# Kernel tuning notes

Measured on AMD Instinct MI355X. Metric: run time of the kernel, lower is better.

Reference implementation:

```python
import jax, jax.numpy as jnp
import numpy as np

E = 512
H = 8
DH = E // H
LN_EPS = 1e-5


def setup_inputs() -> dict:
    key = jax.random.key(0)
    ks = jax.random.split(key, 8)
    s = 1.0 / np.sqrt(E)
    return {
        "query": jax.random.normal(ks[0], (2, 2048, E), jnp.float32),
        "key_value": jax.random.normal(ks[1], (2, 4096, E), jnp.float32),
        "Wq": jax.random.normal(ks[2], (E, E), jnp.float32) * s,
        "bq": jnp.zeros((E,), jnp.float32),
        "Wk": jax.random.normal(ks[3], (E, E), jnp.float32) * s,
        "bk": jnp.zeros((E,), jnp.float32),
        "Wv": jax.random.normal(ks[4], (E, E), jnp.float32) * s,
        "bv": jnp.zeros((E,), jnp.float32),
        "Wo": jax.random.normal(ks[5], (E, E), jnp.float32) * s,
        "bo": jnp.zeros((E,), jnp.float32),
        "ln_gamma": jnp.ones((E,), jnp.float32),
        "ln_beta": jnp.zeros((E,), jnp.float32),
    }


def reference(query, key_value, Wq, bq, Wk, bk, Wv, bv, Wo, bo, ln_gamma, ln_beta):
    B, Lq, _ = query.shape
    Lk = key_value.shape[1]
    # Projections (torch Linear: x @ W.T + b)
    q = (query @ Wq.T + bq).reshape(B, Lq, H, DH)
    k = (key_value @ Wk.T + bk).reshape(B, Lk, H, DH)
    v = (key_value @ Wv.T + bv).reshape(B, Lk, H, DH)
    scale = 1.0 / np.sqrt(DH).astype(np.float32)
    scores = jnp.einsum("bqhd,bkhd->bhqk", q, k) * scale  # [B,H,Lq,Lk]
    attn = jax.nn.softmax(scores, axis=-1)
    ctx = jnp.einsum("bhqk,bkhd->bqhd", attn, v).reshape(B, Lq, E)
    attn_out = ctx @ Wo.T + bo
    # residual + LayerNorm (dropout is identity in eval)
    x = query + attn_out
    mu = jnp.mean(x, axis=-1, keepdims=True)
    var = jnp.mean(jnp.square(x - mu), axis=-1, keepdims=True)
    return (x - mu) * jax.lax.rsqrt(var + LN_EPS) * ln_gamma + ln_beta
```

## Files before the change

### kernel.cpp

```cpp
#include <hip/hip_runtime.h>
#include <hip/hip_bf16.h>

typedef __bf16 bf16;
typedef __bf16 bf16x8 __attribute__((ext_vector_type(8)));
typedef __bf16 bf16x4 __attribute__((ext_vector_type(4)));
typedef float f32x4 __attribute__((ext_vector_type(4)));
typedef float f32x16 __attribute__((ext_vector_type(16)));
typedef unsigned int u32x4 __attribute__((ext_vector_type(4)));

#define MFMA16(a, b, c) __builtin_amdgcn_mfma_f32_16x16x32_bf16((a), (b), (c), 0, 0, 0)
#define MFMA32(a, b, c) __builtin_amdgcn_mfma_f32_32x32x16_bf16((a), (b), (c), 0, 0, 0)

constexpr int LQ = 2048, LK = 4096, E = 512, H = 8, DH = 64;
#define QSCALE 0.1803368801111137f

#if __has_builtin(__builtin_amdgcn_exp2f)
#define EXP2(x) __builtin_amdgcn_exp2f(x)
#else
#define EXP2(x) __expf(0.6931471805599453f * (x))
#endif

__device__ __forceinline__ bf16x8 ld8(const bf16* p) { return *(const bf16x8*)p; }

__global__ __launch_bounds__(256) void cvt4_kernel(
    const float* __restrict__ w0, const float* __restrict__ w1,
    const float* __restrict__ w2, const float* __restrict__ w3,
    bf16* __restrict__ dst) {
  const float* srcs[4] = {w0, w1, w2, w3};
  const float* src = srcs[blockIdx.y];
  bf16* d = dst + (size_t)blockIdx.y * 262144;
  int i = (blockIdx.x * 256 + threadIdx.x) * 4;
  f32x4 v = *(const f32x4*)(src + i);
  bf16x4 o;
  for (int j = 0; j < 4; ++j) o[j] = (bf16)v[j];
  *(bf16x4*)(d + i) = o;
}

__global__ __launch_bounds__(256) void proj_gemm_kernel(
    const float* __restrict__ query, const float* __restrict__ kv,
    const bf16* __restrict__ Wall,
    const float* __restrict__ bq, const float* __restrict__ bk,
    const float* __restrict__ bv,
    bf16* __restrict__ qproj, bf16* __restrict__ kproj, bf16* __restrict__ vt) {
  __shared__ __align__(16) char smem[36864];
  typedef bf16 RowT[72];
  RowT* smA = (RowT*)smem;
  RowT* smB = (RowT*)(smem + 18432);

  const int tid = threadIdx.x;
  const int lane = tid & 63, wave = tid >> 6;
  const int lrow = lane & 15, quad = lane >> 4;
  const int wm = wave & 1, wn = wave >> 1;

  int x = blockIdx.x, z, mt;
  if (x < 32) { z = 0; mt = x; }
  else if (x < 96) { z = 1; mt = x - 32; }
  else { z = 2; mt = x - 96; }
  const float* A = ((z == 0) ? query : kv) + (size_t)mt * 128 * E;
  const bf16* W = Wall + (size_t)z * 262144;
  const float* bias = (z == 0) ? bq : (z == 1) ? bk : bv;
  const int n0 = blockIdx.y * 128;

  const int arow = tid >> 4, acol = tid & 15;
  const int brow = tid >> 3, bcol = tid & 7;

  f32x4 pa[8];
  bf16x8 pb[4];
#define LOAD_T(t)                                                             \
  {                                                                           \
    for (int p = 0; p < 8; ++p)                                               \
      pa[p] = *(const f32x4*)(A + (size_t)(p * 16 + arow) * E + (t) * 64 +    \
                              acol * 4);                                      \
    for (int p = 0; p < 4; ++p)                                               \
      pb[p] = ld8(W + (size_t)(n0 + p * 32 + brow) * E + (t) * 64 + bcol * 8);\
  }
#define STORE_T()                                                             \
  {                                                                           \
    for (int p = 0; p < 8; ++p) {                                             \
      bf16x4 av;                                                              \
      for (int e = 0; e < 4; ++e) av[e] = (bf16)pa[p][e];                     \
      *(bf16x4*)&smA[p * 16 + arow][acol * 4] = av;                           \
    }                                                                         \
    for (int p = 0; p < 4; ++p)                                               \
      *(bf16x8*)&smB[p * 32 + brow][bcol * 8] = pb[p];                        \
  }

  LOAD_T(0);
  STORE_T();
  LOAD_T(1);
  __syncthreads();

  f32x4 acc[4][4] = {};
  for (int t = 0; t < 8; ++t) {
    bf16x8 af[2][4], bfr[2][4];
    for (int ks = 0; ks < 2; ++ks)
      for (int i = 0; i < 4; ++i)
        af[ks][i] = ld8(&smA[wm * 64 + 16 * i + lrow][ks * 32 + quad * 8]);
    for (int ks = 0; ks < 2; ++ks)
      for (int c = 0; c < 4; ++c)
        bfr[ks][c] = ld8(&smB[wn * 64 + 16 * c + lrow][ks * 32 + quad * 8]);
    for (int ks = 0; ks < 2; ++ks)
      for (int i = 0; i < 4; ++i)
        for (int c = 0; c < 4; ++c)
          acc[i][c] = MFMA16(af[ks][i], bfr[ks][c], acc[i][c]);
    if (t < 7) {
      __syncthreads();
      STORE_T();
      if (t < 6) LOAD_T(t + 2);
      __syncthreads();
    }
  }
#undef LOAD_T
#undef STORE_T

  const float qsc = (z == 0) ? QSCALE : 1.f;
  float bvl[4];
  for (int c = 0; c < 4; ++c) bvl[c] = bias[n0 + wn * 64 + 16 * c + lrow];
  __syncthreads();
  bf16* Cs = (bf16*)smem;
  for (int i = 0; i < 4; ++i)
    for (int c = 0; c < 4; ++c)
      for (int r = 0; r < 4; ++r) {
        int row = wm * 64 + 16 * i + 4 * quad + r;
        int col = wn * 64 + 16 * c + lrow;
        bf16 val = (bf16)((acc[i][c][r] + bvl[c]) * qsc);
        if (z < 2) Cs[row * 136 + col] = val;
        else       Cs[col * 136 + row] = val;
      }
  __syncthreads();
  const int rr = tid >> 1, hh = tid & 1;
  if (z == 0) {
    bf16* dstp = qproj + (size_t)(mt * 128 + rr) * E + n0 + hh * 64;
    for (int j = 0; j < 8; ++j)
      *(bf16x8*)(dstp + j * 8) = *(bf16x8*)&Cs[rr * 136 + hh * 64 + j * 8];
  } else if (z == 1) {
    int mtg = mt * 128 + rr;
    int b2 = mtg >> 12, kk = mtg & 4095;
    int t32 = kk >> 5, l31 = kk & 31;
    int bh2 = b2 * 8 + (n0 >> 6) + hh;
    bf16* dstp = kproj + (size_t)bh2 * 262144 + (size_t)t32 * 2048 + l31 * 8;
    for (int j = 0; j < 8; ++j)
      *(bf16x8*)(dstp + j * 256) = *(bf16x8*)&Cs[rr * 136 + hh * 64 + j * 8];
  } else {
    int m0g = mt * 128, b2 = m0g >> 12, kk0 = m0g & 4095;
    int ng = n0 + rr, hd = ng >> 6, d = ng & 63;
    int bh2 = b2 * 8 + hd, dt = d >> 5, l31 = d & 31;
    bf16* dstp = vt + (size_t)bh2 * 262144 + dt * 1024 + l31 * 8;
    for (int j = 0; j < 8; ++j) {
      int kk = kk0 + hh * 64 + 8 * j;
      int t32 = kk >> 5, s = (kk >> 4) & 1, hi2 = (kk >> 3) & 1;
      *(bf16x8*)(dstp + (size_t)t32 * 2048 + s * 512 + hi2 * 256) =
          *(bf16x8*)&Cs[rr * 136 + hh * 64 + j * 8];
    }
  }
}

__global__ __launch_bounds__(256, 2) void attn_kernel(
    const bf16* __restrict__ qp, const bf16* __restrict__ kfg,
    const bf16* __restrict__ vfg, bf16* __restrict__ ctx) {
  const int tid = threadIdx.x;
  const int lane = tid & 63, wave = tid >> 6;
  const int l31 = lane & 31, hi = lane >> 5;
  const int hw = blockIdx.x;
  const int xcd = hw & 7, ii = hw >> 3;
  const int bh = xcd * 2 + (ii >> 5), qt = ii & 31;
  const int b = bh >> 3, h = bh & 7;
  const int q0 = qt * 64;

  __shared__ __align__(16) char smem[34816];

  bf16x8 qf[2][4];
  for (int t = 0; t < 2; ++t)
    for (int st = 0; st < 4; ++st)
      qf[t][st] = ld8(qp + (size_t)(b * LQ + q0 + 32 * t + l31) * E + h * DH +
                      st * 16 + hi * 8);

  float lp[2] = {0.f, 0.f};
  f32x16 acc[2][2] = {};

  const size_t tb = ((size_t)bh * 128 + wave * 32) * 2048;
  const bf16* kb = kfg + tb + hi * 256 + l31 * 8;
  const bf16* vb = vfg + tb + hi * 256 + l31 * 8;

#define LOADT(kf_, vf_, it)                                          \
  {                                                                  \
    const bf16* kp_ = kb + (size_t)(it) * 2048;                      \
    kf_[0] = ld8(kp_);                                               \
    kf_[1] = ld8(kp_ + 512);                                         \
    kf_[2] = ld8(kp_ + 1024);                                        \
    kf_[3] = ld8(kp_ + 1536);                                        \
    const bf16* vp_ = vb + (size_t)(it) * 2048;                      \
    vf_[0] = ld8(vp_);                                               \
    vf_[1] = ld8(vp_ + 512);                                         \
    vf_[2] = ld8(vp_ + 1024);                                        \
    vf_[3] = ld8(vp_ + 1536);                                        \
  }

#define COMPUTE(kf_, vf_)                                            \
  _Pragma("unroll")                                                  \
  for (int t = 0; t < 2; ++t) {                                      \
    f32x16 s_ = {};                                                  \
    __builtin_amdgcn_s_setprio(1);                                   \
    s_ = MFMA32(kf_[0], qf[t][0], s_);                               \
    s_ = MFMA32(kf_[1], qf[t][1], s_);                               \
    s_ = MFMA32(kf_[2], qf[t][2], s_);                               \
    s_ = MFMA32(kf_[3], qf[t][3], s_);                               \
    __builtin_amdgcn_s_setprio(0);                                   \
    unsigned w_[4][2];                                               \
    _Pragma("unroll")                                                \
    for (int t4 = 0; t4 < 4; ++t4)                                   \
      _Pragma("unroll")                                              \
      for (int u = 0; u < 2; ++u) {                                  \
        float e0 = EXP2(s_[4 * t4 + 2 * u]);                         \
        float e1 = EXP2(s_[4 * t4 + 2 * u + 1]);                     \
        lp[t] += e0;                                                 \
        lp[t] += e1;                                                 \
        asm("v_cvt_pk_bf16_f32 %0, %1, %2"                           \
            : "=v"(w_[t4][u])                                        \
            : "v"(e0), "v"(e1));                                     \
      }                                                              \
    bf16x8 paf[2];                                                   \
    _Pragma("unroll")                                                \
    for (int s = 0; s < 2; ++s) {                                    \
      unsigned a0 = w_[2 * s][0], b0 = w_[2 * s + 1][0];             \
      unsigned a1 = w_[2 * s][1], b1 = w_[2 * s + 1][1];             \
      asm("v_permlane32_swap_b32 %0, %1" : "+v"(a0), "+v"(b0));      \
      asm("v_permlane32_swap_b32 %0, %1" : "+v"(a1), "+v"(b1));      \
      u32x4 pw_ = {a0, a1, b0, b1};                                  \
      paf[s] = *(bf16x8*)&pw_;                                       \
    }                                                                \
    __builtin_amdgcn_s_setprio(1);                                   \
    acc[t][0] = MFMA32(paf[0], vf_[0], acc[t][0]);                   \
    acc[t][0] = MFMA32(paf[1], vf_[1], acc[t][0]);                   \
    acc[t][1] = MFMA32(paf[0], vf_[2], acc[t][1]);                   \
    acc[t][1] = MFMA32(paf[1], vf_[3], acc[t][1]);                   \
    __builtin_amdgcn_s_setprio(0);                                   \
  }

  bf16x8 kfA[4], vfA[4], kfB[4], vfB[4];
  LOADT(kfA, vfA, 0);
  for (int it = 0; it < 32; it += 2) {
    LOADT(kfB, vfB, it + 1);
    COMPUTE(kfA, vfA);
    if (it + 2 < 32) LOADT(kfA, vfA, it + 2);
    COMPUTE(kfB, vfB);
  }
#undef LOADT
#undef COMPUTE

  for (int t = 0; t < 2; ++t) lp[t] += __shfl_xor(lp[t], 32);

  float* F = (float*)smem;
  float* Lr = (float*)(smem + 33792);
  if (hi == 0) {
    Lr[wave * 64 + l31] = lp[0];
    Lr[wave * 64 + 32 + l31] = lp[1];
  }
#pragma unroll
  for (int t = 0; t < 2; ++t)
#pragma unroll
    for (int r = 0; r < 16; ++r) {
      int q = 32 * t + (r & 3) + 8 * (r >> 2) + 4 * hi;
      F[(wave * 64 + q) * 33 + l31] = acc[t][0][r];
    }
  __syncthreads();
  const int mq = tid >> 2, d0 = (tid & 3) * 8;
  float ls = Lr[mq] + Lr[64 + mq] + Lr[128 + mq] + Lr[192 + mq];
  const float inv = 1.f / ls;
  {
    float o[8] = {};
#pragma unroll
    for (int w2 = 0; w2 < 4; ++w2) {
      const float* Fr = &F[(w2 * 64 + mq) * 33 + d0];
      for (int j = 0; j < 8; ++j) o[j] += Fr[j];
    }
    bf16x8 ov;
    for (int j = 0; j < 8; ++j) ov[j] = (bf16)(o[j] * inv);
    *(bf16x8*)(ctx + (size_t)(b * LQ + q0 + mq) * E + h * DH + d0) = ov;
  }
  __syncthreads();
#pragma unroll
  for (int t = 0; t < 2; ++t)
#pragma unroll
    for (int r = 0; r < 16; ++r) {
      int q = 32 * t + (r & 3) + 8 * (r >> 2) + 4 * hi;
      F[(wave * 64 + q) * 33 + l31] = acc[t][1][r];
    }
  __syncthreads();
  {
    float o[8] = {};
#pragma unroll
    for (int w2 = 0; w2 < 4; ++w2) {
      const float* Fr = &F[(w2 * 64 + mq) * 33 + d0];
      for (int j = 0; j < 8; ++j) o[j] += Fr[j];
    }
    bf16x8 ov;
    for (int j = 0; j < 8; ++j) ov[j] = (bf16)(o[j] * inv);
    *(bf16x8*)(ctx + (size_t)(b * LQ + q0 + mq) * E + h * DH + 32 + d0) = ov;
  }
}

__global__ __launch_bounds__(256) void outgemm_kernel(
    const bf16* __restrict__ Cx, const bf16* __restrict__ Wo,
    float* __restrict__ y) {
  __shared__ bf16 smA[2][128][72];
  __shared__ bf16 smB[2][128][72];
  const int tid = threadIdx.x;
  const int lane = tid & 63, wave = tid >> 6;
  const int lrow = lane & 15, quad = lane >> 4;
  const int wm = wave & 1, wn = wave >> 1;
  const int m0 = blockIdx.x * 128, n0 = blockIdx.y * 128;
  const bf16* A = Cx + (size_t)m0 * E;

  const int srow = tid >> 3, schunk = tid & 7;

  bf16x8 pa[4], pb[4];
#define LOAD_T(t)                                                             \
  {                                                                           \
    for (int p = 0; p < 4; ++p)                                               \
      pa[p] = ld8(A + (size_t)(p * 32 + srow) * E + (t) * 64 + schunk * 8);   \
    for (int p = 0; p < 4; ++p)                                               \
      pb[p] = ld8(Wo + (size_t)(n0 + p * 32 + srow) * E + (t) * 64 +          \
                  schunk * 8);                                                \
  }
#define STORE_T(bs)                                                           \
  {                                                                           \
    for (int p = 0; p < 4; ++p)                                               \
      *(bf16x8*)&smA[bs][p * 32 + srow][schunk * 8] = pa[p];                  \
    for (int p = 0; p < 4; ++p)                                               \
      *(bf16x8*)&smB[bs][p * 32 + srow][schunk * 8] = pb[p];                  \
  }

  LOAD_T(0);
  STORE_T(0);
  LOAD_T(1);
  __syncthreads();

  f32x4 acc[4][4] = {};
  for (int t = 0; t < 8; ++t) {
    const int bs = t & 1;
    bf16x8 af[2][4], bfr[2][4];
    for (int ks = 0; ks < 2; ++ks)
      for (int i = 0; i < 4; ++i)
        af[ks][i] = ld8(&smA[bs][wm * 64 + 16 * i + lrow][ks * 32 + quad * 8]);
    for (int ks = 0; ks < 2; ++ks)
      for (int c = 0; c < 4; ++c)
        bfr[ks][c] = ld8(&smB[bs][wn * 64 + 16 * c + lrow][ks * 32 + quad * 8]);
    for (int ks = 0; ks < 2; ++ks)
      for (int i = 0; i < 4; ++i)
        for (int c = 0; c < 4; ++c)
          acc[i][c] = MFMA16(af[ks][i], bfr[ks][c], acc[i][c]);
    if (t < 7) {
      STORE_T(bs ^ 1);
      if (t < 6) LOAD_T(t + 2);
    }
    __syncthreads();
  }
#undef LOAD_T
#undef STORE_T

  for (int i = 0; i < 4; ++i)
    for (int c = 0; c < 4; ++c)
      for (int r = 0; r < 4; ++r) {
        int row = m0 + wm * 64 + 16 * i + 4 * quad + r;
        int col = n0 + wn * 64 + 16 * c + lrow;
        y[(size_t)row * E + col] = acc[i][c][r];
      }
}

__global__ __launch_bounds__(256) void ln_kernel(
    const float* __restrict__ y, const float* __restrict__ resid,
    const float* __restrict__ bo, const float* __restrict__ gamma,
    const float* __restrict__ beta, float* __restrict__ out) {
  const int tid = threadIdx.x;
  const int lane = tid & 63, wave = tid >> 6;
  const int row = blockIdx.x * 4 + wave;
  const int c0 = lane * 8;

  const float* yr = y + (size_t)row * E + c0;
  const float* rr = resid + (size_t)row * E + c0;
  f32x4 y0 = *(const f32x4*)yr, y1 = *(const f32x4*)(yr + 4);
  f32x4 r0 = *(const f32x4*)rr, r1 = *(const f32x4*)(rr + 4);
  f32x4 b0 = *(const f32x4*)(bo + c0), b1 = *(const f32x4*)(bo + c0 + 4);

  float xv[8];
  float s1 = 0.f, s2 = 0.f;
  for (int j = 0; j < 4; ++j) {
    xv[j] = y0[j] + r0[j] + b0[j];
    xv[4 + j] = y1[j] + r1[j] + b1[j];
  }
  for (int j = 0; j < 8; ++j) {
    s1 += xv[j];
    s2 += xv[j] * xv[j];
  }
  for (int off = 1; off < 64; off <<= 1) {
    s1 += __shfl_xor(s1, off);
    s2 += __shfl_xor(s2, off);
  }
  const float mean = s1 * (1.f / 512.f);
  const float var = s2 * (1.f / 512.f) - mean * mean;
  const float rstd = rsqrtf(var + 1e-5f);

  f32x4 g0 = *(const f32x4*)(gamma + c0), g1 = *(const f32x4*)(gamma + c0 + 4);
  f32x4 t0 = *(const f32x4*)(beta + c0), t1 = *(const f32x4*)(beta + c0 + 4);
  f32x4 o0, o1;
  for (int j = 0; j < 4; ++j) {
    o0[j] = (xv[j] - mean) * rstd * g0[j] + t0[j];
    o1[j] = (xv[4 + j] - mean) * rstd * g1[j] + t1[j];
  }
  float* op = out + (size_t)row * E + c0;
  *(f32x4*)op = o0;
  *(f32x4*)(op + 4) = o1;
}

extern "C" void kernel_launch(void* const* d_in, const int* in_sizes, int n_in,
                              void* d_out, int out_size, void* d_ws, size_t ws_size,
                              hipStream_t stream) {
  const float* query     = (const float*)d_in[0];
  const float* key_value = (const float*)d_in[1];
  const float* Wq = (const float*)d_in[2];
  const float* bq = (const float*)d_in[3];
  const float* Wk = (const float*)d_in[4];
  const float* bk = (const float*)d_in[5];
  const float* Wv = (const float*)d_in[6];
  const float* bv = (const float*)d_in[7];
  const float* Wo = (const float*)d_in[8];
  const float* bo = (const float*)d_in[9];
  const float* gamma = (const float*)d_in[10];
  const float* beta  = (const float*)d_in[11];
  float* out = (float*)d_out;

  bf16* Wb    = (bf16*)d_ws;
  bf16* Wob   = Wb + (size_t)3 * 262144;
  bf16* qproj = Wb + (size_t)4 * 262144;
  bf16* kproj = qproj + (size_t)4096 * 512;
  bf16* vt    = kproj + (size_t)8192 * 512;
  float* y    = (float*)(vt + (size_t)8192 * 512);

  cvt4_kernel<<<dim3(256, 4), 256, 0, stream>>>(Wq, Wk, Wv, Wo, Wb);
  proj_gemm_kernel<<<dim3(160, 4), 256, 0, stream>>>(
      query, key_value, Wb, bq, bk, bv, qproj, kproj, vt);
  attn_kernel<<<512, 256, 0, stream>>>(qproj, kproj, vt, qproj );
  outgemm_kernel<<<dim3(32, 4), 256, 0, stream>>>(qproj, Wob, y);
  ln_kernel<<<1024, 256, 0, stream>>>(y, query, bo, gamma, beta, out);
}
```

Measured before the change: 167.3 us.

## Pre-swizzle weights into MFMA fragment layout and load B directly from global

The weight conversion kernel now writes bf16 weights in an MFMA-fragment-ordered layout so that each lane can load its B operand straight from global memory into registers. This removes the B shared-memory staging in both projection and output GEMMs. The projection GEMM gains double-buffered A tiles with one barrier per iteration and a 3-block occupancy hint. The output GEMM halves its M tile to 64 rows to double the grid size. The trade-off is more global/L2 traffic for weights, since each wave re-reads its B fragments instead of sharing them through LDS.

```diff
diff --git a/kernel.cpp b/kernel.cpp
--- a/kernel.cpp
+++ b/kernel.cpp
@@ -22,21 +22,28 @@
 
 __device__ __forceinline__ bf16x8 ld8(const bf16* p) { return *(const bf16x8*)p; }
 
-__global__ __launch_bounds__(256) void cvt4_kernel(
+__global__ __launch_bounds__(256) void cvt4f_kernel(
     const float* __restrict__ w0, const float* __restrict__ w1,
     const float* __restrict__ w2, const float* __restrict__ w3,
     bf16* __restrict__ dst) {
+  int gid = blockIdx.x * 256 + threadIdx.x;
+  int z = gid >> 15;
+  int rem = gid & 32767;
+  int row = rem >> 6, cc = rem & 63;
   const float* srcs[4] = {w0, w1, w2, w3};
-  const float* src = srcs[blockIdx.y];
-  bf16* d = dst + (size_t)blockIdx.y * 262144;
-  int i = (blockIdx.x * 256 + threadIdx.x) * 4;
-  f32x4 v = *(const f32x4*)(src + i);
-  bf16x4 o;
-  for (int j = 0; j < 4; ++j) o[j] = (bf16)v[j];
-  *(bf16x4*)(d + i) = o;
-}
-
-__global__ __launch_bounds__(256) void proj_gemm_kernel(
+  const float* s = srcs[z] + row * 512 + cc * 8;
+  f32x4 v0 = *(const f32x4*)s, v1 = *(const f32x4*)(s + 4);
+  bf16x8 o;
+  for (int j = 0; j < 4; ++j) {
+    o[j] = (bf16)v0[j];
+    o[4 + j] = (bf16)v1[j];
+  }
+  int n16 = row >> 4, lrow = row & 15, k32 = cc >> 2, quad = cc & 3;
+  int slot = (n16 * 16 + k32) * 64 + quad * 16 + lrow;
+  *(bf16x8*)(dst + (size_t)z * 262144 + (size_t)slot * 8) = o;
+}
+
+__global__ __launch_bounds__(256, 3) void proj_gemm_kernel(
     const float* __restrict__ query, const float* __restrict__ kv,
     const bf16* __restrict__ Wall,
     const float* __restrict__ bq, const float* __restrict__ bk,
@@ -44,8 +51,8 @@
     bf16* __restrict__ qproj, bf16* __restrict__ kproj, bf16* __restrict__ vt) {
   __shared__ __align__(16) char smem[36864];
   typedef bf16 RowT[72];
-  RowT* smA = (RowT*)smem;
-  RowT* smB = (RowT*)(smem + 18432);
+  RowT* smA0 = (RowT*)smem;
+  RowT* smA1 = (RowT*)(smem + 18432);
 
   const int tid = threadIdx.x;
   const int lane = tid & 63, wave = tid >> 6;
@@ -57,66 +64,67 @@
   else if (x < 96) { z = 1; mt = x - 32; }
   else { z = 2; mt = x - 96; }
   const float* A = ((z == 0) ? query : kv) + (size_t)mt * 128 * E;
-  const bf16* W = Wall + (size_t)z * 262144;
   const float* bias = (z == 0) ? bq : (z == 1) ? bk : bv;
   const int n0 = blockIdx.y * 128;
 
+  const bf16* wb = Wall + (size_t)z * 262144 + (size_t)lane * 8;
+  const int n16b = (n0 >> 4) + wn * 4;
+
   const int arow = tid >> 4, acol = tid & 15;
-  const int brow = tid >> 3, bcol = tid & 7;
 
   f32x4 pa[8];
-  bf16x8 pb[4];
-#define LOAD_T(t)                                                             \
+  bf16x8 bfr[2][4];
+#define LOAD_A(t)                                                             \
+  for (int p = 0; p < 8; ++p)                                                 \
+    pa[p] = *(const f32x4*)(A + (size_t)(p * 16 + arow) * E + (t) * 64 +      \
+                            acol * 4);
+#define STORE_A(bs)                                                           \
   {                                                                           \
-    for (int p = 0; p < 8; ++p)                                               \
-      pa[p] = *(const f32x4*)(A + (size_t)(p * 16 + arow) * E + (t) * 64 +    \
-                              acol * 4);                                      \
-    for (int p = 0; p < 4; ++p)                                               \
-      pb[p] = ld8(W + (size_t)(n0 + p * 32 + brow) * E + (t) * 64 + bcol * 8);\
-  }
-#define STORE_T()                                                             \
-  {                                                                           \
+    RowT* sm_ = (bs) ? smA1 : smA0;                                           \
     for (int p = 0; p < 8; ++p) {                                             \
       bf16x4 av;                                                              \
       for (int e = 0; e < 4; ++e) av[e] = (bf16)pa[p][e];                     \
-      *(bf16x4*)&smA[p * 16 + arow][acol * 4] = av;                           \
+      *(bf16x4*)&sm_[p * 16 + arow][acol * 4] = av;                           \
     }                                                                         \
-    for (int p = 0; p < 4; ++p)                                               \
-      *(bf16x8*)&smB[p * 32 + brow][bcol * 8] = pb[p];                        \
-  }
-
-  LOAD_T(0);
-  STORE_T();
-  LOAD_T(1);
+  }
+#define LOAD_B(t)                                                             \
+  for (int ks = 0; ks < 2; ++ks)                                              \
+    for (int c = 0; c < 4; ++c)                                               \
+      bfr[ks][c] =                                                            \
+          ld8(wb + (size_t)((n16b + c) * 16 + 2 * (t) + ks) * 512);
+
+  LOAD_A(0);
+  STORE_A(0);
+  LOAD_A(1);
+  LOAD_B(0);
   __syncthreads();
 
   f32x4 acc[4][4] = {};
   for (int t = 0; t < 8; ++t) {
-    bf16x8 af[2][4], bfr[2][4];
+    const int bs = t & 1;
+    RowT* sm_ = bs ? smA1 : smA0;
+    bf16x8 af[2][4];
     for (int ks = 0; ks < 2; ++ks)
       for (int i = 0; i < 4; ++i)
-        af[ks][i] = ld8(&smA[wm * 64 + 16 * i + lrow][ks * 32 + quad * 8]);
-    for (int ks = 0; ks < 2; ++ks)
-      for (int c = 0; c < 4; ++c)
-        bfr[ks][c] = ld8(&smB[wn * 64 + 16 * c + lrow][ks * 32 + quad * 8]);
+        af[ks][i] = ld8(&sm_[wm * 64 + 16 * i + lrow][ks * 32 + quad * 8]);
     for (int ks = 0; ks < 2; ++ks)
       for (int i = 0; i < 4; ++i)
         for (int c = 0; c < 4; ++c)
           acc[i][c] = MFMA16(af[ks][i], bfr[ks][c], acc[i][c]);
     if (t < 7) {
-      __syncthreads();
-      STORE_T();
-      if (t < 6) LOAD_T(t + 2);
-      __syncthreads();
-    }
-  }
-#undef LOAD_T
-#undef STORE_T
+      LOAD_B(t + 1);
+      STORE_A(bs ^ 1);
+      if (t < 6) LOAD_A(t + 2);
+    }
+    __syncthreads();
+  }
+#undef LOAD_A
+#undef STORE_A
+#undef LOAD_B
 
   const float qsc = (z == 0) ? QSCALE : 1.f;
   float bvl[4];
   for (int c = 0; c < 4; ++c) bvl[c] = bias[n0 + wn * 64 + 16 * c + lrow];
-  __syncthreads();
   bf16* Cs = (bf16*)smem;
   for (int i = 0; i < 4; ++i)
     for (int c = 0; c < 4; ++c)
@@ -301,68 +309,71 @@
 }
 
 __global__ __launch_bounds__(256) void outgemm_kernel(
-    const bf16* __restrict__ Cx, const bf16* __restrict__ Wo,
+    const bf16* __restrict__ Cx, const bf16* __restrict__ Wof,
     float* __restrict__ y) {
-  __shared__ bf16 smA[2][128][72];
-  __shared__ bf16 smB[2][128][72];
+  __shared__ bf16 smA[2][64][72];
   const int tid = threadIdx.x;
   const int lane = tid & 63, wave = tid >> 6;
   const int lrow = lane & 15, quad = lane >> 4;
   const int wm = wave & 1, wn = wave >> 1;
-  const int m0 = blockIdx.x * 128, n0 = blockIdx.y * 128;
+  const int m0 = blockIdx.x * 64, n0 = blockIdx.y * 128;
   const bf16* A = Cx + (size_t)m0 * E;
 
-  const int srow = tid >> 3, schunk = tid & 7;
-
-  bf16x8 pa[4], pb[4];
-#define LOAD_T(t)                                                             \
+  const int srow = tid >> 2, sc0 = (tid & 3) * 16;
+  const bf16* wb = Wof + (size_t)lane * 8;
+  const int n16b = (n0 >> 4) + wn * 4;
+
+  bf16x8 pa1, pa2;
+  bf16x8 bfr[2][4];
+#define LOAD_A(t)                                                             \
   {                                                                           \
-    for (int p = 0; p < 4; ++p)                                               \
-      pa[p] = ld8(A + (size_t)(p * 32 + srow) * E + (t) * 64 + schunk * 8);   \
-    for (int p = 0; p < 4; ++p)                                               \
-      pb[p] = ld8(Wo + (size_t)(n0 + p * 32 + srow) * E + (t) * 64 +          \
-                  schunk * 8);                                                \
-  }
-#define STORE_T(bs)                                                           \
+    const bf16* ap_ = A + (size_t)srow * E + (t) * 64 + sc0;                  \
+    pa1 = ld8(ap_);                                                           \
+    pa2 = ld8(ap_ + 8);                                                       \
+  }
+#define STORE_A(bs)                                                           \
   {                                                                           \
-    for (int p = 0; p < 4; ++p)                                               \
-      *(bf16x8*)&smA[bs][p * 32 + srow][schunk * 8] = pa[p];                  \
-    for (int p = 0; p < 4; ++p)                                               \
-      *(bf16x8*)&smB[bs][p * 32 + srow][schunk * 8] = pb[p];                  \
-  }
-
-  LOAD_T(0);
-  STORE_T(0);
-  LOAD_T(1);
-  __syncthreads();
-
-  f32x4 acc[4][4] = {};
+    *(bf16x8*)&smA[bs][srow][sc0] = pa1;                                      \
+    *(bf16x8*)&smA[bs][srow][sc0 + 8] = pa2;                                  \
+  }
+#define LOAD_B(t)                                                             \
+  for (int ks = 0; ks < 2; ++ks)                                              \
+    for (int c = 0; c < 4; ++c)                                               \
+      bfr[ks][c] =                                                            \
+          ld8(wb + (size_t)((n16b + c) * 16 + 2 * (t) + ks) * 512);
+
+  LOAD_A(0);
+  STORE_A(0);
+  LOAD_A(1);
+  LOAD_B(0);
+  __syncthreads();
+
+  f32x4 acc[2][4] = {};
   for (int t = 0; t < 8; ++t) {
     const int bs = t & 1;
-    bf16x8 af[2][4], bfr[2][4];
+    bf16x8 af[2][2];
     for (int ks = 0; ks < 2; ++ks)
-      for (int i = 0; i < 4; ++i)
-        af[ks][i] = ld8(&smA[bs][wm * 64 + 16 * i + lrow][ks * 32 + quad * 8]);
+      for (int i = 0; i < 2; ++i)
+        af[ks][i] = ld8(&smA[bs][wm * 32 + 16 * i + lrow][ks * 32 + quad * 8]);
     for (int ks = 0; ks < 2; ++ks)
-      for (int c = 0; c < 4; ++c)
-        bfr[ks][c] = ld8(&smB[bs][wn * 64 + 16 * c + lrow][ks * 32 + quad * 8]);
-    for (int ks = 0; ks < 2; ++ks)
-      for (int i = 0; i < 4; ++i)
+      for (int i = 0; i < 2; ++i)
         for (int c = 0; c < 4; ++c)
           acc[i][c] = MFMA16(af[ks][i], bfr[ks][c], acc[i][c]);
     if (t < 7) {
-      STORE_T(bs ^ 1);
-      if (t < 6) LOAD_T(t + 2);
+      LOAD_B(t + 1);
+      STORE_A(bs ^ 1);
+      if (t < 6) LOAD_A(t + 2);
     }
     __syncthreads();
   }
-#undef LOAD_T
-#undef STORE_T
-
-  for (int i = 0; i < 4; ++i)
+#undef LOAD_A
+#undef STORE_A
+#undef LOAD_B
+
+  for (int i = 0; i < 2; ++i)
     for (int c = 0; c < 4; ++c)
       for (int r = 0; r < 4; ++r) {
-        int row = m0 + wm * 64 + 16 * i + 4 * quad + r;
+        int row = m0 + wm * 32 + 16 * i + 4 * quad + r;
         int col = n0 + wn * 64 + 16 * c + lrow;
         y[(size_t)row * E + col] = acc[i][c][r];
       }
@@ -437,10 +448,10 @@
   bf16* vt    = kproj + (size_t)8192 * 512;
   float* y    = (float*)(vt + (size_t)8192 * 512);
 
-  cvt4_kernel<<<dim3(256, 4), 256, 0, stream>>>(Wq, Wk, Wv, Wo, Wb);
+  cvt4f_kernel<<<512, 256, 0, stream>>>(Wq, Wk, Wv, Wo, Wb);
   proj_gemm_kernel<<<dim3(160, 4), 256, 0, stream>>>(
       query, key_value, Wb, bq, bk, bv, qproj, kproj, vt);
   attn_kernel<<<512, 256, 0, stream>>>(qproj, kproj, vt, qproj );
-  outgemm_kernel<<<dim3(32, 4), 256, 0, stream>>>(qproj, Wob, y);
+  outgemm_kernel<<<dim3(64, 4), 256, 0, stream>>>(qproj, Wob, y);
   ln_kernel<<<1024, 256, 0, stream>>>(y, query, bo, gamma, beta, out);
 }
```

Result: faster. 160.3 us (-4.2%).
